# Kernel tuning notes

Hardware: AMD Instinct MI355X
Metric: run time of the kernel (lower is better)

The kernel has to match this reference:

```python
import jax, jax.numpy as jnp
import numpy as np

LATENT, HID = 32, 64
NODE_FEAT, EDGE_FEAT, ENERGY_DIM, STRESS_DIM = 4, 3, 2, 9
B, N, E = 256, 200000, 1500000


def _lin(key, fan_in, fan_out):
    kw, kb = jax.random.split(key)
    s = 1.0 / np.sqrt(fan_in)
    return (jax.random.uniform(kw, (fan_in, fan_out), jnp.float32, -s, s),
            jax.random.uniform(kb, (fan_out,), jnp.float32, -s, s))


def setup_inputs() -> dict:
    key = jax.random.key(0)
    ks = jax.random.split(key, 16)
    z = jax.random.normal(ks[0], (B, LATENT), jnp.float32)
    node_emb = jax.random.normal(ks[1], (N, 2 * HID), jnp.float32)
    graph_id = jnp.sort(jax.random.randint(ks[2], (N,), 0, B))
    src = jax.random.randint(ks[3], (E,), 0, N)
    dst = jax.random.randint(ks[4], (E,), 0, N)
    lp_w, lp_b = _lin(ks[5], LATENT, 2 * HID)            # latent_proj
    nep_w, nep_b = _lin(ks[6], 2 * HID, 2 * HID)          # node_emb_proj
    nd1_w, nd1_b = _lin(ks[7], 2 * HID, HID)              # node_decoder L1
    nd2_w, nd2_b = _lin(ks[8], HID, NODE_FEAT)            # node_decoder L2
    ed1_w, ed1_b = _lin(ks[9], 4 * HID, HID)              # edge_decoder L1
    ed2_w, ed2_b = _lin(ks[10], HID, EDGE_FEAT)           # edge_decoder L2
    en1_w, en1_b = _lin(ks[11], LATENT, HID)              # energy L1
    en2_w, en2_b = _lin(ks[12], HID, ENERGY_DIM)          # energy L2
    st1_w, st1_b = _lin(ks[13], LATENT, HID)              # stress L1
    st2_w, st2_b = _lin(ks[14], HID, STRESS_DIM)          # stress L2
    return dict(z=z, node_emb=node_emb, graph_id=graph_id, src=src, dst=dst,
                lp_w=lp_w, lp_b=lp_b, nep_w=nep_w, nep_b=nep_b,
                nd1_w=nd1_w, nd1_b=nd1_b, nd2_w=nd2_w, nd2_b=nd2_b,
                ed1_w=ed1_w, ed1_b=ed1_b, ed2_w=ed2_w, ed2_b=ed2_b,
                en1_w=en1_w, en1_b=en1_b, en2_w=en2_w, en2_b=en2_b,
                st1_w=st1_w, st1_b=st1_b, st2_w=st2_w, st2_b=st2_b)


def reference(z, node_emb, graph_id, src, dst,
              lp_w, lp_b, nep_w, nep_b, nd1_w, nd1_b, nd2_w, nd2_b,
              ed1_w, ed1_b, ed2_w, ed2_b, en1_w, en1_b, en2_w, en2_b,
              st1_w, st1_b, st2_w, st2_b):
    # latent_proj + per-graph broadcast (gather replaces the Python loop)
    z_proj = jax.nn.relu(z @ lp_w + lp_b)            # [B, 2H]
    z_expanded = z_proj[graph_id]                    # [N, 2H]
    # node reconstruction (dropout is identity in eval)
    nep = jax.nn.relu(node_emb @ nep_w + nep_b)      # [N, 2H]
    h = z_expanded + nep
    recon_node = jax.nn.relu(h @ nd1_w + nd1_b) @ nd2_w + nd2_b    # [N, 4]
    # edge reconstruction: gather-concat + small MLP
    edge_input = jnp.concatenate([z_expanded[src], z_expanded[dst]], axis=1)  # [E, 4H]
    recon_edge = jax.nn.relu(edge_input @ ed1_w + ed1_b) @ ed2_w + ed2_b       # [E, 3]
    # graph-level predictors
    pred_energy = jax.nn.relu(z @ en1_w + en1_b) @ en2_w + en2_b   # [B, 2]
    pred_stress = jax.nn.relu(z @ st1_w + st1_b) @ st2_w + st2_b   # [B, 9]
    return recon_node, recon_edge, pred_energy, pred_stress
```

## Files before the change

### kernel.cpp

```cpp
#include <hip/hip_runtime.h>
#include <hip/hip_bf16.h>

#define LATENT 32
#define HID 64
#define NB 256
#define NN 200000
#define NE 1500000
#define TWOH 128

#define OUT_NODE_OFF   0
#define OUT_EDGE_OFF   (NN * 4)
#define OUT_ENERGY_OFF (OUT_EDGE_OFF + NE * 3)
#define OUT_STRESS_OFF (OUT_ENERGY_OFF + NB * 2)

#define WS_ZPROJ 0
#define WS_ZC    (WS_ZPROJ + NB*TWOH)
#define WS_P1    (WS_ZC + NB*HID)
#define WS_P2    (WS_P1 + NB*HID)
#define WS_T4    (WS_P2 + NB*HID)
#define WS_W1T   (WS_T4 + NB*NB*4)
#define WS_W2T   (WS_W1T + 8192)

typedef _Float16 half8 __attribute__((ext_vector_type(8)));
typedef _Float16 half4 __attribute__((ext_vector_type(4)));
typedef float f32x4 __attribute__((ext_vector_type(4)));

#define MT 64
#define NTILES (NN / MT)
#define EDGE_BLOCKS ((NE / 4 + 255) / 256)
#define SWZ(r) (((r) & 15) << 3)

__global__ void precompute_kernel(
    const float* __restrict__ z,
    const float* __restrict__ lp_w, const float* __restrict__ lp_b,
    const float* __restrict__ nd1_w,
    const float* __restrict__ ed1_w,
    const float* __restrict__ en1_w, const float* __restrict__ en1_b,
    const float* __restrict__ en2_w, const float* __restrict__ en2_b,
    const float* __restrict__ st1_w, const float* __restrict__ st1_b,
    const float* __restrict__ st2_w, const float* __restrict__ st2_b,
    const float* __restrict__ nep_w,
    float* __restrict__ z_proj, float* __restrict__ zc,
    float* __restrict__ P1, float* __restrict__ P2,
    _Float16* __restrict__ w1T, _Float16* __restrict__ w2T,
    float* __restrict__ out_energy, float* __restrict__ out_stress)
{
    const int t = threadIdx.x;

    if (blockIdx.x >= NB) {
        const int i = (blockIdx.x - NB) * 256 + t;
        if (i < TWOH * TWOH) {
            const int n = i >> 7, k = i & 127;
            w1T[i] = (_Float16)nep_w[k * TWOH + n];
        }
        if (i < HID * TWOH) {
            const int n = i >> 7, k = i & 127;
            w2T[i] = (_Float16)nd1_w[k * HID + n];
        }
        return;
    }

    const int b = blockIdx.x;
    __shared__ float zrow[LATENT];
    __shared__ float zp[TWOH];
    __shared__ float h_en[HID];
    __shared__ float h_st[HID];

    if (t < LATENT) zrow[t] = z[b * LATENT + t];
    __syncthreads();

    if (t < TWOH) {
        float a = lp_b[t];
        #pragma unroll
        for (int k = 0; k < LATENT; ++k)
            a = fmaf(zrow[k], lp_w[k * TWOH + t], a);
        a = fmaxf(a, 0.f);
        zp[t] = a;
        z_proj[b * TWOH + t] = a;
    }
    if (t < HID) {
        float ae = en1_b[t];
        float as = st1_b[t];
        #pragma unroll
        for (int k = 0; k < LATENT; ++k) {
            ae = fmaf(zrow[k], en1_w[k * HID + t], ae);
            as = fmaf(zrow[k], st1_w[k * HID + t], as);
        }
        h_en[t] = fmaxf(ae, 0.f);
        h_st[t] = fmaxf(as, 0.f);
    }
    __syncthreads();

    if (t < HID) {
        float a = 0.f, p1 = 0.f, p2 = 0.f;
        #pragma unroll 8
        for (int k = 0; k < TWOH; ++k) {
            const float zk = zp[k];
            a  = fmaf(zk, nd1_w[k * HID + t], a);
            p1 = fmaf(zk, ed1_w[k * HID + t], p1);
            p2 = fmaf(zk, ed1_w[(TWOH + k) * HID + t], p2);
        }
        zc[b * HID + t] = a;
        P1[b * HID + t] = p1;
        P2[b * HID + t] = p2;
    }
    if (t < 2) {
        float a = en2_b[t];
        #pragma unroll 8
        for (int k = 0; k < HID; ++k) a = fmaf(h_en[k], en2_w[k * 2 + t], a);
        out_energy[b * 2 + t] = a;
    }
    if (t >= 16 && t < 25) {
        const int j = t - 16;
        float a = st2_b[j];
        #pragma unroll 8
        for (int k = 0; k < HID; ++k) a = fmaf(h_st[k], st2_w[k * 9 + j], a);
        out_stress[b * 9 + j] = a;
    }
}

__global__ void edge_table_kernel(
    const float* __restrict__ P1, const float* __restrict__ P2,
    const float* __restrict__ ed1_b,
    const float* __restrict__ ed2_w, const float* __restrict__ ed2_b,
    float4* __restrict__ T4)
{
    const int gs = blockIdx.x;
    const int t  = threadIdx.x;

    __shared__ float p1s[HID];
    __shared__ float w2s[HID * 3];
    __shared__ float b2s[3];

    if (t < HID) p1s[t] = P1[gs * HID + t] + ed1_b[t];
    if (t >= 64 && t < 64 + HID * 3) w2s[t - 64] = ed2_w[t - 64];
    if (t < 3) b2s[t] = ed2_b[t];
    __syncthreads();

    float o0 = b2s[0], o1 = b2s[1], o2 = b2s[2];
    const f32x4* __restrict__ p2 = reinterpret_cast<const f32x4*>(&P2[t * HID]);
    #pragma unroll 4
    for (int k4 = 0; k4 < 16; ++k4) {
        const f32x4 pv = p2[k4];
        #pragma unroll
        for (int j = 0; j < 4; ++j) {
            const int k = k4 * 4 + j;
            const float h = fmaxf(p1s[k] + pv[j], 0.f);
            o0 = fmaf(h, w2s[k * 3 + 0], o0);
            o1 = fmaf(h, w2s[k * 3 + 1], o1);
            o2 = fmaf(h, w2s[k * 3 + 2], o2);
        }
    }
    T4[gs * NB + t] = make_float4(o0, o1, o2, 0.f);
}

__global__ __launch_bounds__(256, 3)
void node_edge_kernel(
    const float* __restrict__ node_emb,
    const int*   __restrict__ graph_id,
    const _Float16* __restrict__ w1T,
    const float* __restrict__ nep_b,
    const _Float16* __restrict__ w2T,
    const float* __restrict__ nd1_b,
    const float* __restrict__ nd2_w, const float* __restrict__ nd2_b,
    const float* __restrict__ zc,
    const int* __restrict__ src, const int* __restrict__ dst,
    const float4* __restrict__ T4,
    float* __restrict__ out_node, float* __restrict__ out_edge)
{
    const int tid = threadIdx.x;
    const int bid = blockIdx.x;

    if (bid >= NTILES) {
        const int e0 = ((bid - NTILES) * 256 + tid) * 4;
        if (e0 >= NE) return;
        const int4 s4 = *reinterpret_cast<const int4*>(&src[e0]);
        const int4 d4 = *reinterpret_cast<const int4*>(&dst[e0]);
        const int ss[4] = {s4.x, s4.y, s4.z, s4.w};
        const int dd[4] = {d4.x, d4.y, d4.z, d4.w};
        float o[12];
        #pragma unroll
        for (int j = 0; j < 4; ++j) {
            const int gs = graph_id[ss[j]];
            const int gd = graph_id[dd[j]];
            const float4 tv = T4[gs * NB + gd];
            o[j * 3 + 0] = tv.x; o[j * 3 + 1] = tv.y; o[j * 3 + 2] = tv.z;
        }
        float4* outp = reinterpret_cast<float4*>(&out_edge[(size_t)e0 * 3]);
        outp[0] = make_float4(o[0], o[1], o[2],  o[3]);
        outp[1] = make_float4(o[4], o[5], o[6],  o[7]);
        outp[2] = make_float4(o[8], o[9], o[10], o[11]);
        return;
    }

    __shared__ _Float16 nepL[MT * TWOH];
    __shared__ float    partL[4 * MT * 4];
    __shared__ int      gidL[MT];

    const int wv   = tid >> 6;
    const int lane = tid & 63;
    const int lrow = lane & 15;
    const int kg   = lane >> 4;
    const size_t nbase = (size_t)bid * MT;

    if (tid < MT) gidL[tid] = graph_id[nbase + tid];

    half8 w1A[2][4];
    #pragma unroll
    for (int cht = 0; cht < 2; ++cht)
        #pragma unroll
        for (int kb = 0; kb < 4; ++kb)
            w1A[cht][kb] = *reinterpret_cast<const half8*>(
                &w1T[(wv * 32 + cht * 16 + lrow) * TWOH + kb * 32 + kg * 8]);
    half8 w2A[4];
    #pragma unroll
    for (int kb = 0; kb < 4; ++kb)
        w2A[kb] = *reinterpret_cast<const half8*>(
            &w2T[(wv * 16 + lrow) * TWOH + kb * 32 + kg * 8]);

    f32x4 b1r[2], b2r, w3r[4];
    #pragma unroll
    for (int cht = 0; cht < 2; ++cht)
        b1r[cht] = *reinterpret_cast<const f32x4*>(&nep_b[wv * 32 + cht * 16 + kg * 4]);
    b2r = *reinterpret_cast<const f32x4*>(&nd1_b[wv * 16 + kg * 4]);
    #pragma unroll
    for (int j = 0; j < 4; ++j)
        w3r[j] = *reinterpret_cast<const f32x4*>(&nd2_w[(wv * 16 + kg * 4 + j) * 4]);
    const float b3 = nd2_b[tid & 3];

    f32x4 acc1[2][4];
    #pragma unroll
    for (int cht = 0; cht < 2; ++cht)
        #pragma unroll
        for (int nt = 0; nt < 4; ++nt)
            acc1[cht][nt] = (f32x4){0.f, 0.f, 0.f, 0.f};

    #pragma unroll
    for (int nt = 0; nt < 4; ++nt) {
        const float* ep = node_emb + (nbase + nt * 16 + lrow) * TWOH + kg * 8;
        f32x4 u[4], v[4];
        #pragma unroll
        for (int kb = 0; kb < 4; ++kb) {
            u[kb] = *reinterpret_cast<const f32x4*>(ep + kb * 32);
            v[kb] = *reinterpret_cast<const f32x4*>(ep + kb * 32 + 4);
        }
        #pragma unroll
        for (int kb = 0; kb < 4; ++kb) {
            half8 h;
            h[0] = (_Float16)u[kb][0]; h[1] = (_Float16)u[kb][1];
            h[2] = (_Float16)u[kb][2]; h[3] = (_Float16)u[kb][3];
            h[4] = (_Float16)v[kb][0]; h[5] = (_Float16)v[kb][1];
            h[6] = (_Float16)v[kb][2]; h[7] = (_Float16)v[kb][3];
            acc1[0][nt] = __builtin_amdgcn_mfma_f32_16x16x32_f16(
                w1A[0][kb], h, acc1[0][nt], 0, 0, 0);
            acc1[1][nt] = __builtin_amdgcn_mfma_f32_16x16x32_f16(
                w1A[1][kb], h, acc1[1][nt], 0, 0, 0);
        }
    }
    #pragma unroll
    for (int cht = 0; cht < 2; ++cht)
        #pragma unroll
        for (int nt = 0; nt < 4; ++nt) {
            const int node = nt * 16 + lrow;
            const int ch = wv * 32 + cht * 16 + kg * 4;
            half4 h;
            #pragma unroll
            for (int j = 0; j < 4; ++j)
                h[j] = (_Float16)fmaxf(acc1[cht][nt][j] + b1r[cht][j], 0.f);
            *reinterpret_cast<half4*>(&nepL[(node * TWOH + ch) ^ SWZ(node)]) = h;
        }
    __syncthreads();

    f32x4 acc2[4];
    #pragma unroll
    for (int nt = 0; nt < 4; ++nt) acc2[nt] = (f32x4){0.f, 0.f, 0.f, 0.f};

    #pragma unroll
    for (int nt = 0; nt < 4; ++nt) {
        #pragma unroll
        for (int kb = 0; kb < 4; ++kb) {
            const int node = nt * 16 + lrow;
            const int e = node * TWOH + kb * 32 + kg * 8;
            const half8 nB = *reinterpret_cast<const half8*>(&nepL[e ^ SWZ(node)]);
            acc2[nt] = __builtin_amdgcn_mfma_f32_16x16x32_f16(
                w2A[kb], nB, acc2[nt], 0, 0, 0);
        }
    }

    f32x4 p[4];
    #pragma unroll
    for (int nt = 0; nt < 4; ++nt) {
        const int node = nt * 16 + lrow;
        const int g = gidL[node];
        const f32x4 z4 = *reinterpret_cast<const f32x4*>(
            &zc[(size_t)g * HID + wv * 16 + kg * 4]);
        f32x4 t4;
        #pragma unroll
        for (int j = 0; j < 4; ++j)
            t4[j] = fmaxf(acc2[nt][j] + b2r[j] + z4[j], 0.f);
        f32x4 pp = t4[0] * w3r[0];
        pp += t4[1] * w3r[1];
        pp += t4[2] * w3r[2];
        pp += t4[3] * w3r[3];
        p[nt] = pp;
    }
    #pragma unroll
    for (int nt = 0; nt < 4; ++nt) {
        #pragma unroll
        for (int j = 0; j < 4; ++j) {
            p[nt][j] += __shfl_xor(p[nt][j], 16, 64);
            p[nt][j] += __shfl_xor(p[nt][j], 32, 64);
        }
    }
    if (lane < 16) {
        #pragma unroll
        for (int nt = 0; nt < 4; ++nt)
            *reinterpret_cast<f32x4*>(
                &partL[(wv * MT + nt * 16 + lrow) * 4]) = p[nt];
    }
    __syncthreads();

    {
        const int node = tid >> 2;
        const int o    = tid & 3;
        const int ix = node * 4 + o;
        const float s = partL[ix] + partL[256 + ix] +
                        partL[512 + ix] + partL[768 + ix] + b3;
        out_node[(nbase + node) * 4 + o] = s;
    }
}

extern "C" void kernel_launch(void* const* d_in, const int* in_sizes, int n_in,
                              void* d_out, int out_size, void* d_ws, size_t ws_size,
                              hipStream_t stream)
{
    const float* z        = (const float*)d_in[0];
    const float* node_emb = (const float*)d_in[1];
    const int*   graph_id = (const int*)  d_in[2];
    const int*   src      = (const int*)  d_in[3];
    const int*   dst      = (const int*)  d_in[4];
    const float* lp_w  = (const float*)d_in[5];
    const float* lp_b  = (const float*)d_in[6];
    const float* nep_w = (const float*)d_in[7];
    const float* nep_b = (const float*)d_in[8];
    const float* nd1_w = (const float*)d_in[9];
    const float* nd1_b = (const float*)d_in[10];
    const float* nd2_w = (const float*)d_in[11];
    const float* nd2_b = (const float*)d_in[12];
    const float* ed1_w = (const float*)d_in[13];
    const float* ed1_b = (const float*)d_in[14];
    const float* ed2_w = (const float*)d_in[15];
    const float* ed2_b = (const float*)d_in[16];
    const float* en1_w = (const float*)d_in[17];
    const float* en1_b = (const float*)d_in[18];
    const float* en2_w = (const float*)d_in[19];
    const float* en2_b = (const float*)d_in[20];
    const float* st1_w = (const float*)d_in[21];
    const float* st1_b = (const float*)d_in[22];
    const float* st2_w = (const float*)d_in[23];
    const float* st2_b = (const float*)d_in[24];

    float* out = (float*)d_out;
    float* out_node   = out + OUT_NODE_OFF;
    float* out_edge   = out + OUT_EDGE_OFF;
    float* out_energy = out + OUT_ENERGY_OFF;
    float* out_stress = out + OUT_STRESS_OFF;

    float* ws     = (float*)d_ws;
    float* z_proj = ws + WS_ZPROJ;
    float* zc     = ws + WS_ZC;
    float* P1     = ws + WS_P1;
    float* P2     = ws + WS_P2;
    float4* T4    = (float4*)(ws + WS_T4);
    _Float16* w1T = (_Float16*)(ws + WS_W1T);
    _Float16* w2T = (_Float16*)(ws + WS_W2T);

    precompute_kernel<<<NB + 64, 256, 0, stream>>>(
        z, lp_w, lp_b, nd1_w, ed1_w,
        en1_w, en1_b, en2_w, en2_b, st1_w, st1_b, st2_w, st2_b, nep_w,
        z_proj, zc, P1, P2, w1T, w2T, out_energy, out_stress);

    edge_table_kernel<<<NB, NB, 0, stream>>>(P1, P2, ed1_b, ed2_w, ed2_b, T4);

    node_edge_kernel<<<NTILES + EDGE_BLOCKS, 256, 0, stream>>>(
        node_emb, graph_id, w1T, nep_b, w2T, nd1_b, nd2_w, nd2_b, zc,
        src, dst, T4, out_node, out_edge);
}
```

Measured before the change: 282.1 us.

## Restructure node MLP to per-wave 16-node tiles with LDS-resident weights and shuffles

The node path is restructured. Each 512-thread block stages the full swizzled fp16 weight matrices in LDS, and each wave handles two 16-node tiles on its own, computing all output channels. The layer-1 output is passed to layer 2 through cross-lane shuffles instead of an LDS round trip with block barriers. Per-node partial sums are reduced inside the wave rather than across waves. The aim is to remove block-level syncs and the per-block re-read of weights into registers. In exchange, each block must first load 48KB of weights, and the edge blocks grow to 512 threads.

Result: faster. 255.0 us (-9.6%).

```diff
diff --git a/kernel.cpp b/kernel.cpp
--- a/kernel.cpp
+++ b/kernel.cpp
@@ -24,11 +24,13 @@
 typedef _Float16 half8 __attribute__((ext_vector_type(8)));
 typedef _Float16 half4 __attribute__((ext_vector_type(4)));
 typedef float f32x4 __attribute__((ext_vector_type(4)));
-
-#define MT 64
-#define NTILES (NN / MT)
-#define EDGE_BLOCKS ((NE / 4 + 255) / 256)
-#define SWZ(r) (((r) & 15) << 3)
+typedef int i32x2 __attribute__((ext_vector_type(2)));
+typedef int i32x4 __attribute__((ext_vector_type(4)));
+
+#define WTILES 12500
+#define TPW 2
+#define NODE_BLK 782
+#define EDGE_BLK 733
 
 __global__ void precompute_kernel(
     const float* __restrict__ z,
@@ -42,7 +44,7 @@
     const float* __restrict__ nep_w,
     float* __restrict__ z_proj, float* __restrict__ zc,
     float* __restrict__ P1, float* __restrict__ P2,
-    _Float16* __restrict__ w1T, _Float16* __restrict__ w2T,
+    _Float16* __restrict__ w1s, _Float16* __restrict__ w2s,
     float* __restrict__ out_energy, float* __restrict__ out_stress)
 {
     const int t = threadIdx.x;
@@ -50,12 +52,14 @@
     if (blockIdx.x >= NB) {
         const int i = (blockIdx.x - NB) * 256 + t;
         if (i < TWOH * TWOH) {
-            const int n = i >> 7, k = i & 127;
-            w1T[i] = (_Float16)nep_w[k * TWOH + n];
+            const int ch = i >> 7, k = i & 127;
+            const int dst = ch * TWOH + (((k >> 3) ^ (ch & 7)) << 3) + (k & 7);
+            w1s[dst] = (_Float16)nep_w[k * TWOH + ch];
         }
         if (i < HID * TWOH) {
-            const int n = i >> 7, k = i & 127;
-            w2T[i] = (_Float16)nd1_w[k * HID + n];
+            const int ch = i >> 7, k = i & 127;
+            const int dst = ch * TWOH + (((k >> 3) ^ (ch & 7)) << 3) + (k & 7);
+            w2s[dst] = (_Float16)nd1_w[k * HID + ch];
         }
         return;
     }
@@ -129,11 +133,11 @@
     const int t  = threadIdx.x;
 
     __shared__ float p1s[HID];
-    __shared__ float w2s[HID * 3];
+    __shared__ float w2s_[HID * 3];
     __shared__ float b2s[3];
 
     if (t < HID) p1s[t] = P1[gs * HID + t] + ed1_b[t];
-    if (t >= 64 && t < 64 + HID * 3) w2s[t - 64] = ed2_w[t - 64];
+    if (t >= 64 && t < 64 + HID * 3) w2s_[t - 64] = ed2_w[t - 64];
     if (t < 3) b2s[t] = ed2_b[t];
     __syncthreads();
 
@@ -146,21 +150,21 @@
         for (int j = 0; j < 4; ++j) {
             const int k = k4 * 4 + j;
             const float h = fmaxf(p1s[k] + pv[j], 0.f);
-            o0 = fmaf(h, w2s[k * 3 + 0], o0);
-            o1 = fmaf(h, w2s[k * 3 + 1], o1);
-            o2 = fmaf(h, w2s[k * 3 + 2], o2);
+            o0 = fmaf(h, w2s_[k * 3 + 0], o0);
+            o1 = fmaf(h, w2s_[k * 3 + 1], o1);
+            o2 = fmaf(h, w2s_[k * 3 + 2], o2);
         }
     }
     T4[gs * NB + t] = make_float4(o0, o1, o2, 0.f);
 }
 
-__global__ __launch_bounds__(256, 3)
+__global__ __launch_bounds__(512, 4)
 void node_edge_kernel(
     const float* __restrict__ node_emb,
     const int*   __restrict__ graph_id,
-    const _Float16* __restrict__ w1T,
+    const _Float16* __restrict__ w1s,
     const float* __restrict__ nep_b,
-    const _Float16* __restrict__ w2T,
+    const _Float16* __restrict__ w2s,
     const float* __restrict__ nd1_b,
     const float* __restrict__ nd2_w, const float* __restrict__ nd2_b,
     const float* __restrict__ zc,
@@ -171,8 +175,8 @@
     const int tid = threadIdx.x;
     const int bid = blockIdx.x;
 
-    if (bid >= NTILES) {
-        const int e0 = ((bid - NTILES) * 256 + tid) * 4;
+    if (bid >= NODE_BLK) {
+        const int e0 = ((bid - NODE_BLK) * 512 + tid) * 4;
         if (e0 >= NE) return;
         const int4 s4 = *reinterpret_cast<const int4*>(&src[e0]);
         const int4 d4 = *reinterpret_cast<const int4*>(&dst[e0]);
@@ -193,140 +197,133 @@
         return;
     }
 
-    __shared__ _Float16 nepL[MT * TWOH];
-    __shared__ float    partL[4 * MT * 4];
-    __shared__ int      gidL[MT];
+    __shared__ _Float16 w1L[TWOH * TWOH];
+    __shared__ _Float16 w2L[HID * TWOH];
+    __shared__ float    b1L[TWOH];
+    __shared__ float    b2L[HID];
+    __shared__ float    w3L[HID * 4];
+
+    {
+        const uint4* g1 = reinterpret_cast<const uint4*>(w1s);
+        uint4* l1 = reinterpret_cast<uint4*>(w1L);
+        #pragma unroll
+        for (int i = 0; i < 4; ++i) l1[tid + 512 * i] = g1[tid + 512 * i];
+        const uint4* g2 = reinterpret_cast<const uint4*>(w2s);
+        uint4* l2 = reinterpret_cast<uint4*>(w2L);
+        #pragma unroll
+        for (int i = 0; i < 2; ++i) l2[tid + 512 * i] = g2[tid + 512 * i];
+        if (tid < TWOH)    b1L[tid] = nep_b[tid];
+        if (tid < HID)     b2L[tid] = nd1_b[tid];
+        if (tid < HID * 4) w3L[tid] = nd2_w[tid];
+    }
+    __syncthreads();
 
     const int wv   = tid >> 6;
     const int lane = tid & 63;
     const int lrow = lane & 15;
     const int kg   = lane >> 4;
-    const size_t nbase = (size_t)bid * MT;
-
-    if (tid < MT) gidL[tid] = graph_id[nbase + tid];
-
-    half8 w1A[2][4];
+    const int hi   = kg >> 1;
+    const int srcA = lrow | ((kg & 1) << 5);
+    const int srcB = srcA | 16;
+
     #pragma unroll
-    for (int cht = 0; cht < 2; ++cht)
-        #pragma unroll
-        for (int kb = 0; kb < 4; ++kb)
-            w1A[cht][kb] = *reinterpret_cast<const half8*>(
-                &w1T[(wv * 32 + cht * 16 + lrow) * TWOH + kb * 32 + kg * 8]);
-    half8 w2A[4];
-    #pragma unroll
-    for (int kb = 0; kb < 4; ++kb)
-        w2A[kb] = *reinterpret_cast<const half8*>(
-            &w2T[(wv * 16 + lrow) * TWOH + kb * 32 + kg * 8]);
-
-    f32x4 b1r[2], b2r, w3r[4];
-    #pragma unroll
-    for (int cht = 0; cht < 2; ++cht)
-        b1r[cht] = *reinterpret_cast<const f32x4*>(&nep_b[wv * 32 + cht * 16 + kg * 4]);
-    b2r = *reinterpret_cast<const f32x4*>(&nd1_b[wv * 16 + kg * 4]);
-    #pragma unroll
-    for (int j = 0; j < 4; ++j)
-        w3r[j] = *reinterpret_cast<const f32x4*>(&nd2_w[(wv * 16 + kg * 4 + j) * 4]);
-    const float b3 = nd2_b[tid & 3];
-
-    f32x4 acc1[2][4];
-    #pragma unroll
-    for (int cht = 0; cht < 2; ++cht)
-        #pragma unroll
-        for (int nt = 0; nt < 4; ++nt)
-            acc1[cht][nt] = (f32x4){0.f, 0.f, 0.f, 0.f};
-
-    #pragma unroll
-    for (int nt = 0; nt < 4; ++nt) {
-        const float* ep = node_emb + (nbase + nt * 16 + lrow) * TWOH + kg * 8;
-        f32x4 u[4], v[4];
+    for (int tt = 0; tt < TPW; ++tt) {
+        const int tile = (bid * 8 + wv) * TPW + tt;
+        if (tile >= WTILES) break;
+        const size_t nb16 = (size_t)tile * 16;
+        const int node = (int)nb16 + lrow;
+
+        const int g = graph_id[node];
+        f32x4 zv[4];
+        #pragma unroll
+        for (int c2 = 0; c2 < 4; ++c2)
+            zv[c2] = *reinterpret_cast<const f32x4*>(
+                &zc[(size_t)g * HID + c2 * 16 + kg * 4]);
+
+        f32x4 acc1[8];
+        #pragma unroll
+        for (int cht = 0; cht < 8; ++cht)
+            acc1[cht] = *reinterpret_cast<const f32x4*>(&b1L[cht * 16 + kg * 4]);
+
         #pragma unroll
         for (int kb = 0; kb < 4; ++kb) {
-            u[kb] = *reinterpret_cast<const f32x4*>(ep + kb * 32);
-            v[kb] = *reinterpret_cast<const f32x4*>(ep + kb * 32 + 4);
-        }
-        #pragma unroll
-        for (int kb = 0; kb < 4; ++kb) {
+            const float* ep = node_emb + (size_t)node * TWOH + kb * 32 + kg * 8;
+            const f32x4 u = *reinterpret_cast<const f32x4*>(ep);
+            const f32x4 v = *reinterpret_cast<const f32x4*>(ep + 4);
             half8 h;
-            h[0] = (_Float16)u[kb][0]; h[1] = (_Float16)u[kb][1];
-            h[2] = (_Float16)u[kb][2]; h[3] = (_Float16)u[kb][3];
-            h[4] = (_Float16)v[kb][0]; h[5] = (_Float16)v[kb][1];
-            h[6] = (_Float16)v[kb][2]; h[7] = (_Float16)v[kb][3];
-            acc1[0][nt] = __builtin_amdgcn_mfma_f32_16x16x32_f16(
-                w1A[0][kb], h, acc1[0][nt], 0, 0, 0);
-            acc1[1][nt] = __builtin_amdgcn_mfma_f32_16x16x32_f16(
-                w1A[1][kb], h, acc1[1][nt], 0, 0, 0);
-        }
-    }
-    #pragma unroll
-    for (int cht = 0; cht < 2; ++cht)
-        #pragma unroll
-        for (int nt = 0; nt < 4; ++nt) {
-            const int node = nt * 16 + lrow;
-            const int ch = wv * 32 + cht * 16 + kg * 4;
-            half4 h;
+            h[0] = (_Float16)u[0]; h[1] = (_Float16)u[1];
+            h[2] = (_Float16)u[2]; h[3] = (_Float16)u[3];
+            h[4] = (_Float16)v[0]; h[5] = (_Float16)v[1];
+            h[6] = (_Float16)v[2]; h[7] = (_Float16)v[3];
+            const int koff = (((kb * 4 + kg) ^ (lrow & 7)) << 3);
+            #pragma unroll
+            for (int cht = 0; cht < 8; ++cht) {
+                const half8 w = *reinterpret_cast<const half8*>(
+                    &w1L[(cht * 16 + lrow) * TWOH + koff]);
+                acc1[cht] = __builtin_amdgcn_mfma_f32_16x16x32_f16(
+                    w, h, acc1[cht], 0, 0, 0);
+            }
+        }
+
+        half4 vv[8];
+        #pragma unroll
+        for (int cht = 0; cht < 8; ++cht) {
+            half4 hv;
             #pragma unroll
             for (int j = 0; j < 4; ++j)
-                h[j] = (_Float16)fmaxf(acc1[cht][nt][j] + b1r[cht][j], 0.f);
-            *reinterpret_cast<half4*>(&nepL[(node * TWOH + ch) ^ SWZ(node)]) = h;
-        }
-    __syncthreads();
-
-    f32x4 acc2[4];
-    #pragma unroll
-    for (int nt = 0; nt < 4; ++nt) acc2[nt] = (f32x4){0.f, 0.f, 0.f, 0.f};
-
-    #pragma unroll
-    for (int nt = 0; nt < 4; ++nt) {
+                hv[j] = (_Float16)fmaxf(acc1[cht][j], 0.f);
+            vv[cht] = hv;
+        }
+
+        f32x4 acc2[4];
+        #pragma unroll
+        for (int c2 = 0; c2 < 4; ++c2)
+            acc2[c2] = *reinterpret_cast<const f32x4*>(&b2L[c2 * 16 + kg * 4])
+                       + zv[c2];
+
         #pragma unroll
         for (int kb = 0; kb < 4; ++kb) {
-            const int node = nt * 16 + lrow;
-            const int e = node * TWOH + kb * 32 + kg * 8;
-            const half8 nB = *reinterpret_cast<const half8*>(&nepL[e ^ SWZ(node)]);
-            acc2[nt] = __builtin_amdgcn_mfma_f32_16x16x32_f16(
-                w2A[kb], nB, acc2[nt], 0, 0, 0);
-        }
-    }
-
-    f32x4 p[4];
-    #pragma unroll
-    for (int nt = 0; nt < 4; ++nt) {
-        const int node = nt * 16 + lrow;
-        const int g = gidL[node];
-        const f32x4 z4 = *reinterpret_cast<const f32x4*>(
-            &zc[(size_t)g * HID + wv * 16 + kg * 4]);
-        f32x4 t4;
-        #pragma unroll
-        for (int j = 0; j < 4; ++j)
-            t4[j] = fmaxf(acc2[nt][j] + b2r[j] + z4[j], 0.f);
-        f32x4 pp = t4[0] * w3r[0];
-        pp += t4[1] * w3r[1];
-        pp += t4[2] * w3r[2];
-        pp += t4[3] * w3r[3];
-        p[nt] = pp;
-    }
-    #pragma unroll
-    for (int nt = 0; nt < 4; ++nt) {
+            const i32x2 a0 = __builtin_bit_cast(i32x2, vv[2 * kb]);
+            const i32x2 a1 = __builtin_bit_cast(i32x2, vv[2 * kb + 1]);
+            const int A0x = __shfl(a0.x, srcA, 64), A0y = __shfl(a0.y, srcA, 64);
+            const int A1x = __shfl(a1.x, srcA, 64), A1y = __shfl(a1.y, srcA, 64);
+            const int B0x = __shfl(a0.x, srcB, 64), B0y = __shfl(a0.y, srcB, 64);
+            const int B1x = __shfl(a1.x, srcB, 64), B1y = __shfl(a1.y, srcB, 64);
+            i32x4 wp;
+            wp.x = hi ? A1x : A0x;  wp.y = hi ? A1y : A0y;
+            wp.z = hi ? B1x : B0x;  wp.w = hi ? B1y : B0y;
+            const half8 nB = __builtin_bit_cast(half8, wp);
+
+            const int koff = (((kb * 4 + kg) ^ (lrow & 7)) << 3);
+            #pragma unroll
+            for (int c2 = 0; c2 < 4; ++c2) {
+                const half8 w = *reinterpret_cast<const half8*>(
+                    &w2L[(c2 * 16 + lrow) * TWOH + koff]);
+                acc2[c2] = __builtin_amdgcn_mfma_f32_16x16x32_f16(
+                    w, nB, acc2[c2], 0, 0, 0);
+            }
+        }
+
+        f32x4 p = {0.f, 0.f, 0.f, 0.f};
+        #pragma unroll
+        for (int c2 = 0; c2 < 4; ++c2) {
+            #pragma unroll
+            for (int r = 0; r < 4; ++r) {
+                const float tval = fmaxf(acc2[c2][r], 0.f);
+                const f32x4 w3v = *reinterpret_cast<const f32x4*>(
+                    &w3L[(c2 * 16 + kg * 4 + r) * 4]);
+                p += tval * w3v;
+            }
+        }
         #pragma unroll
         for (int j = 0; j < 4; ++j) {
-            p[nt][j] += __shfl_xor(p[nt][j], 16, 64);
-            p[nt][j] += __shfl_xor(p[nt][j], 32, 64);
-        }
-    }
-    if (lane < 16) {
-        #pragma unroll
-        for (int nt = 0; nt < 4; ++nt)
-            *reinterpret_cast<f32x4*>(
-                &partL[(wv * MT + nt * 16 + lrow) * 4]) = p[nt];
-    }
-    __syncthreads();
-
-    {
-        const int node = tid >> 2;
-        const int o    = tid & 3;
-        const int ix = node * 4 + o;
-        const float s = partL[ix] + partL[256 + ix] +
-                        partL[512 + ix] + partL[768 + ix] + b3;
-        out_node[(nbase + node) * 4 + o] = s;
+            p[j] += __shfl_xor(p[j], 16, 64);
+            p[j] += __shfl_xor(p[j], 32, 64);
+        }
+        if (kg == 0) {
+            const f32x4 b3 = *reinterpret_cast<const f32x4*>(&nd2_b[0]);
+            *reinterpret_cast<f32x4*>(&out_node[(size_t)node * 4]) = p + b3;
+        }
     }
 }
 
@@ -372,17 +369,17 @@
     float* P1     = ws + WS_P1;
     float* P2     = ws + WS_P2;
     float4* T4    = (float4*)(ws + WS_T4);
-    _Float16* w1T = (_Float16*)(ws + WS_W1T);
-    _Float16* w2T = (_Float16*)(ws + WS_W2T);
+    _Float16* w1s = (_Float16*)(ws + WS_W1T);
+    _Float16* w2s = (_Float16*)(ws + WS_W2T);
 
     precompute_kernel<<<NB + 64, 256, 0, stream>>>(
         z, lp_w, lp_b, nd1_w, ed1_w,
         en1_w, en1_b, en2_w, en2_b, st1_w, st1_b, st2_w, st2_b, nep_w,
-        z_proj, zc, P1, P2, w1T, w2T, out_energy, out_stress);
+        z_proj, zc, P1, P2, w1s, w2s, out_energy, out_stress);
 
     edge_table_kernel<<<NB, NB, 0, stream>>>(P1, P2, ed1_b, ed2_w, ed2_b, T4);
 
-    node_edge_kernel<<<NTILES + EDGE_BLOCKS, 256, 0, stream>>>(
-        node_emb, graph_id, w1T, nep_b, w2T, nd1_b, nd2_w, nd2_b, zc,
+    node_edge_kernel<<<NODE_BLK + EDGE_BLK, 512, 0, stream>>>(
+        node_emb, graph_id, w1s, nep_b, w2s, nd1_b, nd2_w, nd2_b, zc,
         src, dst, T4, out_node, out_edge);
 }
```
